# Kernel optimization log

Hardware: AMD Instinct MI355X
Metric: run time of the kernel (lower is better)

The kernel has to match this reference:

```python
import jax, jax.numpy as jnp
import numpy as np

B, S, DIM = 1, 2048, 2048
H, KVH = 32, 8
D = DIM // H  # 64


def setup_inputs() -> dict:
    key = jax.random.key(0)
    ks = jax.random.split(key, 10)
    x = jax.random.normal(ks[0], (B, S, DIM), dtype=jnp.float32)
    # RoPE frequencies: theta=10000, per LLaMA
    inv_freq = 1.0 / (10000.0 ** (np.arange(0, D, 2, dtype=np.float32) / D))  # (D/2,)
    angles = np.arange(S, dtype=np.float32)[:, None] * inv_freq[None, :]      # (S, D/2)
    freqs_cos = jnp.asarray(np.cos(angles))
    freqs_sin = jnp.asarray(np.sin(angles))
    # causal mask (1,1,S,S), 1 = keep, 0 = masked
    mask = jnp.tril(jnp.ones((S, S), dtype=jnp.int32))[None, None, :, :]
    w = 0.02
    Wq = jax.random.normal(ks[1], (DIM, H * D), dtype=jnp.float32) * w
    bq = jnp.zeros((H * D,), dtype=jnp.float32)
    Wk = jax.random.normal(ks[2], (DIM, KVH * D), dtype=jnp.float32) * w
    bk = jnp.zeros((KVH * D,), dtype=jnp.float32)
    Wv = jax.random.normal(ks[3], (DIM, KVH * D), dtype=jnp.float32) * w
    bv = jnp.zeros((KVH * D,), dtype=jnp.float32)
    Wo = jax.random.normal(ks[4], (H * D, DIM), dtype=jnp.float32) * w
    bo = jnp.zeros((DIM,), dtype=jnp.float32)
    return {"x": x, "freqs_cos": freqs_cos, "freqs_sin": freqs_sin, "mask": mask,
            "Wq": Wq, "bq": bq, "Wk": Wk, "bk": bk, "Wv": Wv, "bv": bv, "Wo": Wo, "bo": bo}


def _rope(t, cos, sin):
    # t: (B, S, h, D) with D even; rotate consecutive pairs (real form of complex mult)
    tr = t.reshape(*t.shape[:-1], -1, 2)          # (B,S,h,D/2,2)
    c = cos[None, :, None, :]                     # (1,S,1,D/2)
    s = sin[None, :, None, :]
    o0 = tr[..., 0] * c - tr[..., 1] * s
    o1 = tr[..., 0] * s + tr[..., 1] * c
    return jnp.stack([o0, o1], axis=-1).reshape(t.shape)


def reference(x, freqs_cos, freqs_sin, mask, Wq, bq, Wk, bk, Wv, bv, Wo, bo):
    b, s, dim = x.shape
    scale = 1.0 / jnp.sqrt(jnp.asarray(D, dtype=x.dtype))
    q = (x @ Wq + bq).reshape(b, s, H, D)
    k = (x @ Wk + bk).reshape(b, s, KVH, D)
    v = (x @ Wv + bv).reshape(b, s, KVH, D)
    q = _rope(q, freqs_cos, freqs_sin)
    k = _rope(k, freqs_cos, freqs_sin)
    # GQA: repeat kv heads to match query heads
    rep = H // KVH
    k = jnp.repeat(k, rep, axis=2)
    v = jnp.repeat(v, rep, axis=2)
    # to (B, H, S, D)
    q = q.transpose(0, 2, 1, 3)
    k = k.transpose(0, 2, 1, 3)
    v = v.transpose(0, 2, 1, 3)
    scores = jnp.einsum('bhqd,bhkd->bhqk', q, k) * scale   # (B,H,S,S)
    neg = jnp.asarray(jnp.finfo(scores.dtype).min, dtype=scores.dtype)
    scores = jnp.where(mask == 0, neg, scores)
    attn = jax.nn.softmax(scores, axis=-1)
    out = jnp.einsum('bhqk,bhkd->bhqd', attn, v)            # (B,H,S,D)
    out = out.transpose(0, 2, 1, 3).reshape(b, s, H * D)
    return out @ Wo + bo
```

## Files before the change

kernel.cpp:

```cpp
#include <hip/hip_runtime.h>
#include <stdint.h>

#define S_LEN 2048
#define DIM   2048
#define NHEAD 32
#define KVHEAD 8
#define HDIM  64
#define NQKV  3072

typedef __attribute__((ext_vector_type(8))) __bf16 bf16x8;
typedef __attribute__((ext_vector_type(4))) float f32x4;
typedef __attribute__((ext_vector_type(8))) unsigned short u16x8;
typedef __attribute__((ext_vector_type(4))) unsigned int u32x4;

#if __has_builtin(__builtin_amdgcn_exp2f)
#define EXP2F(x) __builtin_amdgcn_exp2f(x)
#else
#define EXP2F(x) exp2f(x)
#endif

__device__ __forceinline__ unsigned short f2bf(float f) {
  unsigned u = __builtin_bit_cast(unsigned, f);
  unsigned r = (u + 0x7FFFu + ((u >> 16) & 1u)) >> 16;
  return (unsigned short)r;
}
__device__ __forceinline__ float bf2f(unsigned short h) {
  unsigned u = ((unsigned)h) << 16;
  return __builtin_bit_cast(float, u);
}

__device__ __forceinline__ void gl_lds16(const void* g, void* l) {
  __builtin_amdgcn_global_load_lds(
      (const __attribute__((address_space(1))) unsigned*)g,
      (__attribute__((address_space(3))) unsigned*)l, 16, 0, 0);
}

__global__ void prep_kernel(const float* __restrict__ x,
                            const float* __restrict__ bq,
                            const float* __restrict__ bk,
                            const float* __restrict__ bv,
                            const float* __restrict__ Wq,
                            const float* __restrict__ Wk,
                            const float* __restrict__ Wv,
                            const float* __restrict__ Wo,
                            unsigned short* __restrict__ xb,
                            unsigned short* __restrict__ WqkvT,
                            unsigned short* __restrict__ WoT,
                            float* __restrict__ bqkv) {
  int idx = blockIdx.x;
  int tid = threadIdx.x;
  if (idx < 10240) {
    __shared__ float t[32][33];
    int bx = idx >> 6, by = idx & 63;
    const float* src; int C, sc, dbase; unsigned short* dst;
    if (bx < 64)      { src = Wq; C = 2048; sc = bx * 32;        dst = WqkvT; dbase = sc; }
    else if (bx < 80) { src = Wk; C = 512;  sc = (bx - 64) * 32; dst = WqkvT; dbase = 2048 + sc; }
    else if (bx < 96) { src = Wv; C = 512;  sc = (bx - 80) * 32; dst = WqkvT; dbase = 2560 + sc; }
    else              { src = Wo; C = 2048; sc = (bx - 96) * 32; dst = WoT;   dbase = sc; }
    int tx = tid & 31, ty = tid >> 5;
#pragma unroll
    for (int j = 0; j < 32; j += 8)
      t[ty + j][tx] = src[(size_t)(by * 32 + ty + j) * C + sc + tx];
    __syncthreads();
#pragma unroll
    for (int j = 0; j < 32; j += 8)
      dst[(size_t)(dbase + ty + j) * 2048 + by * 32 + tx] = f2bf(t[tx][ty + j]);
  } else if (idx < 14336) {
    int i = (idx - 10240) * 256 + tid;
    float4 v = ((const float4*)x)[i];
    ushort4 o;
    o.x = f2bf(v.x); o.y = f2bf(v.y); o.z = f2bf(v.z); o.w = f2bf(v.w);
    ((ushort4*)xb)[i] = o;
  } else {
    int i = (idx - 14336) * 256 + tid;
    if (i < NQKV)
      bqkv[i] = (i < 2048) ? bq[i] : (i < 2560 ? bk[i - 2048] : bv[i - 2560]);
  }
}

__global__ void rope_vt_kernel(unsigned short* __restrict__ qkv,
                               const float* __restrict__ fc,
                               const float* __restrict__ fs,
                               unsigned short* __restrict__ VT) {
  int idx = blockIdx.x;
  int tid = threadIdx.x;
  if (idx < 10240) {
    int i = idx * 256 + tid;
    int row = i / 1280;
    int p   = i - row * 1280;
    int col = (p < 1024) ? (p * 2) : (2048 + (p - 1024) * 2);
    int fi = p & 31;
    float c  = fc[row * 32 + fi];
    float sn = fs[row * 32 + fi];
    unsigned* base = (unsigned*)(qkv + (size_t)row * NQKV + col);
    unsigned v = *base;
    float x0 = bf2f((unsigned short)(v & 0xFFFF));
    float x1 = bf2f((unsigned short)(v >> 16));
    unsigned short o0 = f2bf(x0 * c - x1 * sn);
    unsigned short o1 = f2bf(x0 * sn + x1 * c);
    *base = (unsigned)o0 | ((unsigned)o1 << 16);
  } else {
    __shared__ unsigned short t[32][33];
    int sub = idx - 10240;
    int bx = (sub & 15) * 32;
    int by = (sub >> 4) * 32;
    int tx = tid & 31, ty = tid >> 5;
    const unsigned short* src = qkv + 2560;
#pragma unroll
    for (int j = 0; j < 32; j += 8)
      t[ty + j][tx] = src[(size_t)(by + ty + j) * 3072 + bx + tx];
    __syncthreads();
#pragma unroll
    for (int j = 0; j < 32; j += 8)
      VT[(size_t)(bx + ty + j) * 2048 + by + tx] = t[tx][ty + j];
  }
}

template <int NJ, int OUT_BF16>
__global__ __launch_bounds__(512, 4) void gemm_bt_kernel(
    const unsigned short* __restrict__ A,
    const unsigned short* __restrict__ BT,
    const float* __restrict__ bias,
    void* __restrict__ Cc, int M, int N, int K) {
  constexpr int BUFB = 16384 + NJ * 4096;
  __shared__ char smem[2 * BUFB];
  const int tid = threadIdx.x;
  const int lane = tid & 63;
  const int wid = tid >> 6;
  const int kh = wid >> 2;
  const int wsub = wid & 3;
  const int wm = wsub >> 1, wn = wsub & 1;
  const int rowA0 = blockIdx.x * 128;
  const int rowB0 = blockIdx.y * (32 * NJ);
  const int l15 = lane & 15, l4 = lane >> 4;
  const int kcol = kh * 64 + l4 * 16;

  f32x4 acc[4][NJ];
#pragma unroll
  for (int i = 0; i < 4; i++)
#pragma unroll
    for (int j = 0; j < NJ; j++) acc[i][j] = (f32x4){0.f, 0.f, 0.f, 0.f};

  const int nK = K >> 6;

  auto stage = [&](int buf, int kt) {
    const char* Ab = (const char*)A + ((size_t)rowA0 * K + (size_t)kt * 64) * 2;
    const char* Bb = (const char*)BT + ((size_t)rowB0 * K + (size_t)kt * 64) * 2;
    char* Sb = smem + buf * BUFB;
#pragma unroll
    for (int j = 0; j < 2; ++j) {
      int chunk = wid + 8 * j;
      int o = chunk * 1024 + lane * 16;
      int r = o >> 7;
      int cb = (o & 127) ^ ((r & 7) << 4);
      gl_lds16(Ab + (size_t)r * (K * 2) + cb, Sb + chunk * 1024);
    }
#pragma unroll
    for (int j = 0; j < (NJ + 1) / 2; ++j) {
      int chunk = wid + 8 * j;
      if (chunk < 4 * NJ) {
        int o = chunk * 1024 + lane * 16;
        int r = o >> 7;
        int cb = (o & 127) ^ ((r & 7) << 4);
        gl_lds16(Bb + (size_t)r * (K * 2) + cb, Sb + 16384 + chunk * 1024);
      }
    }
  };

  stage(0, 0);
  int buf = 0;

  for (int kt = 0; kt < nK; ++kt) {
    if (kt + 1 < nK) {
      stage(buf ^ 1, kt + 1);
      asm volatile("s_waitcnt vmcnt(3)" ::: "memory");
    } else {
      asm volatile("s_waitcnt vmcnt(0)" ::: "memory");
    }
    __builtin_amdgcn_s_barrier();
    asm volatile("" ::: "memory");

    bf16x8 af[4], bfr[NJ];
    char* Sb = smem + buf * BUFB;
#pragma unroll
    for (int i = 0; i < 4; i++) {
      int ra = wm * 64 + i * 16 + l15;
      af[i] = *(const bf16x8*)(Sb + ra * 128 + (kcol ^ ((ra & 7) << 4)));
    }
#pragma unroll
    for (int j = 0; j < NJ; j++) {
      int rb = wn * (NJ * 16) + j * 16 + l15;
      bfr[j] = *(const bf16x8*)(Sb + 16384 + rb * 128 + (kcol ^ ((rb & 7) << 4)));
    }
#pragma unroll
    for (int i = 0; i < 4; i++)
#pragma unroll
      for (int j = 0; j < NJ; j++)
        acc[i][j] = __builtin_amdgcn_mfma_f32_16x16x32_bf16(af[i], bfr[j], acc[i][j], 0, 0, 0);
    __builtin_amdgcn_s_barrier();
    asm volatile("" ::: "memory");
    buf ^= 1;
  }

  f32x4* eps = (f32x4*)smem;
  if (kh == 1) {
#pragma unroll
    for (int i = 0; i < 4; i++)
#pragma unroll
      for (int j = 0; j < NJ; j++)
        eps[wsub * (4 * NJ * 64) + (i * NJ + j) * 64 + lane] = acc[i][j];
  }
  __syncthreads();
  if (kh == 0) {
#pragma unroll
    for (int i = 0; i < 4; i++) {
      int row0 = rowA0 + wm * 64 + i * 16 + l4 * 4;
#pragma unroll
      for (int j = 0; j < NJ; j++) {
        f32x4 oth = eps[wsub * (4 * NJ * 64) + (i * NJ + j) * 64 + lane];
        int col = rowB0 + wn * (NJ * 16) + j * 16 + l15;
        float bv_ = bias[col];
#pragma unroll
        for (int r = 0; r < 4; r++) {
          float v = acc[i][j][r] + oth[r] + bv_;
          size_t idx = (size_t)(row0 + r) * N + col;
          if (OUT_BF16) ((unsigned short*)Cc)[idx] = f2bf(v);
          else          ((float*)Cc)[idx] = v;
        }
      }
    }
  }
}

__global__ __launch_bounds__(512, 4) void attn_kernel(
    const unsigned short* __restrict__ qkv,
    const unsigned short* __restrict__ VT,
    unsigned short* __restrict__ O) {
  __shared__ unsigned short Ks[4][64 * 64];
  __shared__ unsigned short VTs[4][64 * 64];

  const int tid = threadIdx.x;
  const int lane = tid & 63;
  const int w = tid >> 6;
  const int l15 = lane & 15, l4 = lane >> 4;
  const int kvh = blockIdx.x & 7;
  const int qt  = 63 - (blockIdx.x >> 3);
  const int h = kvh * 4 + (w >> 1);
  const int qsub = (w & 1) * 16;
  const int nt = (qt >> 1) + 1;
  const int qbase = qt * 32;

  auto issue = [&](int buf, int t) {
    int kvb = t * 64;
    int o = tid << 4;
    int r = o >> 7;
    int cb = (o & 127) ^ ((r & 7) << 4);
    gl_lds16((const char*)qkv + ((size_t)(kvb + r) * NQKV + 2048 + kvh * 64) * 2 + cb,
             (char*)&Ks[buf][0] + o);
    gl_lds16((const char*)VT + ((size_t)(kvh * 64 + r) * S_LEN + kvb) * 2 + cb,
             (char*)&VTs[buf][0] + o);
  };

  bf16x8 qf[2];
  {
    const unsigned short* qrow = qkv + (size_t)(qbase + qsub + l15) * NQKV + h * 64;
#pragma unroll
    for (int kf = 0; kf < 2; ++kf) {
      u16x8 raw = *(const u16x8*)(qrow + kf * 32 + l4 * 8);
      u16x8 sc;
#pragma unroll
      for (int i = 0; i < 8; i++) sc[i] = f2bf(bf2f(raw[i]) * 0.1803368801111f);
      qf[kf] = __builtin_bit_cast(bf16x8, sc);
    }
  }

  f32x4 oacc[4];
  float lsum = 0.f;
#pragma unroll
  for (int d = 0; d < 4; d++) oacc[d] = (f32x4){0.f, 0.f, 0.f, 0.f};

  auto compute_tile = [&](int buf, int kvb, bool domask) {
    f32x4 sacc[4];
#pragma unroll
    for (int nf = 0; nf < 4; nf++) sacc[nf] = (f32x4){0.f, 0.f, 0.f, 0.f};
#pragma unroll
    for (int nf = 0; nf < 4; nf++) {
#pragma unroll
      for (int kf = 0; kf < 2; kf++) {
        int row = nf * 16 + l15;
        bf16x8 kb = *(const bf16x8*)((const char*)&Ks[buf][0] + row * 128 +
                                     ((kf * 64 + l4 * 16) ^ ((row & 7) << 4)));
        sacc[nf] = __builtin_amdgcn_mfma_f32_16x16x32_bf16(kb, qf[kf], sacc[nf], 0, 0, 0);
      }
    }
    if (domask) {
      int qpos = qbase + qsub + l15;
#pragma unroll
      for (int nf = 0; nf < 4; nf++) {
#pragma unroll
        for (int r = 0; r < 4; r++) {
          int kvpos = kvb + nf * 16 + l4 * 4 + r;
          if (kvpos > qpos) sacc[nf][r] = -3.0e38f;
        }
      }
    }
#pragma unroll
    for (int nf = 0; nf < 4; nf++)
#pragma unroll
      for (int r = 0; r < 4; r++) {
        float p = EXP2F(sacc[nf][r]);
        lsum += p;
        sacc[nf][r] = p;
      }
    unsigned wds[4][2];
#pragma unroll
    for (int nf = 0; nf < 4; nf++)
#pragma unroll
      for (int m = 0; m < 2; m++)
        asm("v_cvt_pk_bf16_f32 %0, %1, %2"
            : "=v"(wds[nf][m]) : "v"(sacc[nf][2 * m]), "v"(sacc[nf][2 * m + 1]));
    bf16x8 paf[2];
#pragma unroll
    for (int kc = 0; kc < 2; kc++) {
      unsigned a0 = wds[2 * kc][0], b0 = wds[2 * kc + 1][0];
      unsigned a1 = wds[2 * kc][1], b1 = wds[2 * kc + 1][1];
      asm("v_permlane32_swap_b32 %0, %1" : "+v"(a0), "+v"(b0));
      asm("v_permlane16_swap_b32 %0, %1" : "+v"(a0), "+v"(b0));
      asm("v_permlane32_swap_b32 %0, %1" : "+v"(a1), "+v"(b1));
      asm("v_permlane16_swap_b32 %0, %1" : "+v"(a1), "+v"(b1));
      u32x4 afu = (u32x4){a0, a1, b0, b1};
      paf[kc] = __builtin_bit_cast(bf16x8, afu);
    }
#pragma unroll
    for (int kc = 0; kc < 2; kc++) {
#pragma unroll
      for (int df = 0; df < 4; df++) {
        int row = df * 16 + l15;
        bf16x8 vb = *(const bf16x8*)((const char*)&VTs[buf][0] + row * 128 +
                                     ((kc * 64 + l4 * 16) ^ ((row & 7) << 4)));
        oacc[df] = __builtin_amdgcn_mfma_f32_16x16x32_bf16(paf[kc], vb, oacc[df], 0, 0, 0);
      }
    }
  };

  issue(0, 0);
  if (nt > 1) issue(1, 1);
  if (nt > 2) issue(2, 2);
  if (nt > 3) issue(3, 3);

  int t = 0;
  for (; t + 3 < nt; t += 2) {
    asm volatile("s_waitcnt vmcnt(4)" ::: "memory");
    __builtin_amdgcn_s_barrier();
    asm volatile("" ::: "memory");
    __builtin_amdgcn_s_setprio(1);
    compute_tile(t & 3, t * 64, false);
    compute_tile((t + 1) & 3, (t + 1) * 64, false);
    __builtin_amdgcn_s_setprio(0);
    __builtin_amdgcn_s_barrier();
    asm volatile("" ::: "memory");
    if (t + 4 < nt) issue((t + 4) & 3, t + 4);
    if (t + 5 < nt) issue((t + 5) & 3, t + 5);
  }
  int rem = nt - t;
  if (rem == 3) {
    asm volatile("s_waitcnt vmcnt(2)" ::: "memory");
    __builtin_amdgcn_s_barrier();
    asm volatile("" ::: "memory");
    __builtin_amdgcn_s_setprio(1);
    compute_tile(t & 3, t * 64, false);
    compute_tile((t + 1) & 3, (t + 1) * 64, false);
    __builtin_amdgcn_s_setprio(0);
    asm volatile("s_waitcnt vmcnt(0)" ::: "memory");
    __builtin_amdgcn_s_barrier();
    asm volatile("" ::: "memory");
    compute_tile((t + 2) & 3, (t + 2) * 64, true);
  } else if (rem == 2) {
    asm volatile("s_waitcnt vmcnt(0)" ::: "memory");
    __builtin_amdgcn_s_barrier();
    asm volatile("" ::: "memory");
    __builtin_amdgcn_s_setprio(1);
    compute_tile(t & 3, t * 64, false);
    compute_tile((t + 1) & 3, (t + 1) * 64, true);
    __builtin_amdgcn_s_setprio(0);
  } else {
    asm volatile("s_waitcnt vmcnt(0)" ::: "memory");
    __builtin_amdgcn_s_barrier();
    asm volatile("" ::: "memory");
    compute_tile(t & 3, t * 64, true);
  }

  lsum += __shfl_xor(lsum, 16, 64);
  lsum += __shfl_xor(lsum, 32, 64);

#pragma unroll
  for (int r = 0; r < 4; r++) {
    float inv = 1.0f / __shfl(lsum, l4 * 4 + r, 16);
    int qpos = qbase + qsub + l4 * 4 + r;
#pragma unroll
    for (int df = 0; df < 4; df++)
      O[(size_t)qpos * DIM + h * 64 + df * 16 + l15] = f2bf(oacc[df][r] * inv);
  }
}

extern "C" void kernel_launch(void* const* d_in, const int* in_sizes, int n_in,
                              void* d_out, int out_size, void* d_ws, size_t ws_size,
                              hipStream_t stream) {
  const float* x  = (const float*)d_in[0];
  const float* fc = (const float*)d_in[1];
  const float* fs = (const float*)d_in[2];
  const float* Wq = (const float*)d_in[4];
  const float* bq = (const float*)d_in[5];
  const float* Wk = (const float*)d_in[6];
  const float* bk = (const float*)d_in[7];
  const float* Wv = (const float*)d_in[8];
  const float* bv = (const float*)d_in[9];
  const float* Wo = (const float*)d_in[10];
  const float* bo = (const float*)d_in[11];
  float* out = (float*)d_out;

  char* ws = (char*)d_ws;
  unsigned short* xb    = (unsigned short*)(ws + 0);
  unsigned short* WqkvT = (unsigned short*)(ws + 8388608);
  unsigned short* WoT   = (unsigned short*)(ws + 20971520);
  float*          bqkv  = (float*)(ws + 29360128);
  unsigned short* qkv   = (unsigned short*)(ws + 29372416);
  unsigned short* VT    = WqkvT;
  unsigned short* attn  = xb;

  prep_kernel<<<14348, 256, 0, stream>>>(x, bq, bk, bv, Wq, Wk, Wv, Wo,
                                         xb, WqkvT, WoT, bqkv);
  gemm_bt_kernel<3, 1><<<dim3(16, 32), 512, 0, stream>>>(xb, WqkvT, bqkv, qkv, 2048, 3072, 2048);
  rope_vt_kernel<<<11264, 256, 0, stream>>>(qkv, fc, fs, VT);
  attn_kernel<<<512, 512, 0, stream>>>(qkv, VT, attn);
  gemm_bt_kernel<2, 0><<<dim3(16, 32), 512, 0, stream>>>(attn, WoT, bo, out, 2048, 2048, 2048);
}
```

Measured before the change: 215.1 us.

## Fuse RoPE into QKV GEMM epilogue and triple-buffer output projection GEMM

Applies the rotary embedding inside the QKV GEMM epilogue, using a lane shuffle to get the paired column, so the separate RoPE read-modify-write pass over Q and K is removed; the V transpose becomes its own small kernel. The output projection GEMM switches to a three-stage shared-memory pipeline with one barrier per k-step. This trades an extra launch-free memory pass for more epilogue work and larger shared memory use, which may reduce occupancy.

```diff
diff --git a/kernel.cpp b/kernel.cpp
--- a/kernel.cpp
+++ b/kernel.cpp
@@ -78,52 +78,34 @@
   }
 }
 
-__global__ void rope_vt_kernel(unsigned short* __restrict__ qkv,
-                               const float* __restrict__ fc,
-                               const float* __restrict__ fs,
-                               unsigned short* __restrict__ VT) {
-  int idx = blockIdx.x;
+__global__ void vt_kernel(const unsigned short* __restrict__ qkv,
+                          unsigned short* __restrict__ VT) {
+  __shared__ unsigned short t[32][33];
+  int sub = blockIdx.x;
   int tid = threadIdx.x;
-  if (idx < 10240) {
-    int i = idx * 256 + tid;
-    int row = i / 1280;
-    int p   = i - row * 1280;
-    int col = (p < 1024) ? (p * 2) : (2048 + (p - 1024) * 2);
-    int fi = p & 31;
-    float c  = fc[row * 32 + fi];
-    float sn = fs[row * 32 + fi];
-    unsigned* base = (unsigned*)(qkv + (size_t)row * NQKV + col);
-    unsigned v = *base;
-    float x0 = bf2f((unsigned short)(v & 0xFFFF));
-    float x1 = bf2f((unsigned short)(v >> 16));
-    unsigned short o0 = f2bf(x0 * c - x1 * sn);
-    unsigned short o1 = f2bf(x0 * sn + x1 * c);
-    *base = (unsigned)o0 | ((unsigned)o1 << 16);
-  } else {
-    __shared__ unsigned short t[32][33];
-    int sub = idx - 10240;
-    int bx = (sub & 15) * 32;
-    int by = (sub >> 4) * 32;
-    int tx = tid & 31, ty = tid >> 5;
-    const unsigned short* src = qkv + 2560;
-#pragma unroll
-    for (int j = 0; j < 32; j += 8)
-      t[ty + j][tx] = src[(size_t)(by + ty + j) * 3072 + bx + tx];
-    __syncthreads();
-#pragma unroll
-    for (int j = 0; j < 32; j += 8)
-      VT[(size_t)(bx + ty + j) * 2048 + by + tx] = t[tx][ty + j];
-  }
-}
-
-template <int NJ, int OUT_BF16>
+  int bx = (sub & 15) * 32;
+  int by = (sub >> 4) * 32;
+  int tx = tid & 31, ty = tid >> 5;
+  const unsigned short* src = qkv + 2560;
+#pragma unroll
+  for (int j = 0; j < 32; j += 8)
+    t[ty + j][tx] = src[(size_t)(by + ty + j) * 3072 + bx + tx];
+  __syncthreads();
+#pragma unroll
+  for (int j = 0; j < 32; j += 8)
+    VT[(size_t)(bx + ty + j) * 2048 + by + tx] = t[tx][ty + j];
+}
+
+template <int NJ, int OUT_BF16, int ROPE, int NBUF>
 __global__ __launch_bounds__(512, 4) void gemm_bt_kernel(
     const unsigned short* __restrict__ A,
     const unsigned short* __restrict__ BT,
     const float* __restrict__ bias,
+    const float* __restrict__ fc,
+    const float* __restrict__ fs,
     void* __restrict__ Cc, int M, int N, int K) {
   constexpr int BUFB = 16384 + NJ * 4096;
-  __shared__ char smem[2 * BUFB];
+  __shared__ char smem[NBUF * BUFB];
   const int tid = threadIdx.x;
   const int lane = tid & 63;
   const int wid = tid >> 6;
@@ -167,19 +149,7 @@
     }
   };
 
-  stage(0, 0);
-  int buf = 0;
-
-  for (int kt = 0; kt < nK; ++kt) {
-    if (kt + 1 < nK) {
-      stage(buf ^ 1, kt + 1);
-      asm volatile("s_waitcnt vmcnt(3)" ::: "memory");
-    } else {
-      asm volatile("s_waitcnt vmcnt(0)" ::: "memory");
-    }
-    __builtin_amdgcn_s_barrier();
-    asm volatile("" ::: "memory");
-
+  auto compute = [&](int buf) {
     bf16x8 af[4], bfr[NJ];
     char* Sb = smem + buf * BUFB;
 #pragma unroll
@@ -197,9 +167,37 @@
 #pragma unroll
       for (int j = 0; j < NJ; j++)
         acc[i][j] = __builtin_amdgcn_mfma_f32_16x16x32_bf16(af[i], bfr[j], acc[i][j], 0, 0, 0);
-    __builtin_amdgcn_s_barrier();
-    asm volatile("" ::: "memory");
-    buf ^= 1;
+  };
+
+  if constexpr (NBUF == 2) {
+    stage(0, 0);
+    int buf = 0;
+    for (int kt = 0; kt < nK; ++kt) {
+      if (kt + 1 < nK) {
+        stage(buf ^ 1, kt + 1);
+        asm volatile("s_waitcnt vmcnt(3)" ::: "memory");
+      } else {
+        asm volatile("s_waitcnt vmcnt(0)" ::: "memory");
+      }
+      __builtin_amdgcn_s_barrier();
+      asm volatile("" ::: "memory");
+      compute(buf);
+      __builtin_amdgcn_s_barrier();
+      asm volatile("" ::: "memory");
+      buf ^= 1;
+    }
+  } else {
+    stage(0, 0);
+    if (nK > 1) stage(1, 1);
+    for (int kt = 0; kt < nK; ++kt) {
+      if (kt + 1 < nK) { asm volatile("s_waitcnt vmcnt(3)" ::: "memory"); }
+      else             { asm volatile("s_waitcnt vmcnt(0)" ::: "memory"); }
+      __builtin_amdgcn_s_barrier();
+      asm volatile("" ::: "memory");
+      if (kt + 2 < nK) stage((kt + 2) % 3, kt + 2);
+      compute(kt % 3);
+    }
+    __syncthreads();
   }
 
   f32x4* eps = (f32x4*)smem;
@@ -220,12 +218,31 @@
         f32x4 oth = eps[wsub * (4 * NJ * 64) + (i * NJ + j) * 64 + lane];
         int col = rowB0 + wn * (NJ * 16) + j * 16 + l15;
         float bv_ = bias[col];
+        float vals[4];
+#pragma unroll
+        for (int r = 0; r < 4; r++) vals[r] = acc[i][j][r] + oth[r] + bv_;
+        if (ROPE) {
+          float prt[4];
+#pragma unroll
+          for (int r = 0; r < 4; r++) prt[r] = __shfl_xor(vals[r], 1, 64);
+          if (col < 2560) {
+            int fi = (col & 63) >> 1;
+            bool even = (col & 1) == 0;
+#pragma unroll
+            for (int r = 0; r < 4; r++) {
+              int row = row0 + r;
+              float c = fc[row * 32 + fi];
+              float s = fs[row * 32 + fi];
+              vals[r] = even ? (vals[r] * c - prt[r] * s)
+                             : (prt[r] * s + vals[r] * c);
+            }
+          }
+        }
 #pragma unroll
         for (int r = 0; r < 4; r++) {
-          float v = acc[i][j][r] + oth[r] + bv_;
           size_t idx = (size_t)(row0 + r) * N + col;
-          if (OUT_BF16) ((unsigned short*)Cc)[idx] = f2bf(v);
-          else          ((float*)Cc)[idx] = v;
+          if (OUT_BF16) ((unsigned short*)Cc)[idx] = f2bf(vals[r]);
+          else          ((float*)Cc)[idx] = vals[r];
         }
       }
     }
@@ -430,8 +447,10 @@
 
   prep_kernel<<<14348, 256, 0, stream>>>(x, bq, bk, bv, Wq, Wk, Wv, Wo,
                                          xb, WqkvT, WoT, bqkv);
-  gemm_bt_kernel<3, 1><<<dim3(16, 32), 512, 0, stream>>>(xb, WqkvT, bqkv, qkv, 2048, 3072, 2048);
-  rope_vt_kernel<<<11264, 256, 0, stream>>>(qkv, fc, fs, VT);
+  gemm_bt_kernel<3, 1, 1, 2><<<dim3(16, 32), 512, 0, stream>>>(
+      xb, WqkvT, bqkv, fc, fs, qkv, 2048, 3072, 2048);
+  vt_kernel<<<1024, 256, 0, stream>>>(qkv, VT);
   attn_kernel<<<512, 512, 0, stream>>>(qkv, VT, attn);
-  gemm_bt_kernel<2, 0><<<dim3(16, 32), 512, 0, stream>>>(attn, WoT, bo, out, 2048, 2048, 2048);
-}
+  gemm_bt_kernel<2, 0, 0, 3><<<dim3(16, 32), 512, 0, stream>>>(
+      attn, WoT, bo, fc, fs, out, 2048, 2048, 2048);
+}
```

Result: no change. 215.8 us (+0.3%).
